# Performance work log

Hardware: AMD Instinct MI355X
Metric: run time of the kernel (lower is better)

The kernel has to match this reference:

```python
import jax, jax.numpy as jnp
import numpy as np

I4_CLIP = 7.0
NUM_HEADS = 16
NUM_KV_HEADS = 4
HEAD_DIM = 64
ROPE_BASE = 10000.0


def fake_quant_i4(w):
    # per-row int4 symmetric fake quantization with straight-through estimator
    row_max = jnp.maximum(jnp.max(jnp.abs(w), axis=-1, keepdims=True), 1e-8)
    scale = row_max / I4_CLIP
    w_deq = jnp.clip(jnp.round(w / scale), -I4_CLIP, I4_CLIP) * scale
    return w + jax.lax.stop_gradient(w_deq - w)


def rms_norm(x):
    eps = jnp.asarray(jnp.finfo(x.dtype).eps, x.dtype)
    return x * jax.lax.rsqrt(jnp.mean(x * x, axis=-1, keepdims=True) + eps)


def rope_cos_sin(seqlen, dtype):
    inv_freq = 1.0 / (ROPE_BASE ** (jnp.arange(0, HEAD_DIM, 2, dtype=jnp.float32) / HEAD_DIM))
    freqs = jnp.outer(jnp.arange(seqlen, dtype=jnp.float32), inv_freq)  # [S, hd/2]
    return jnp.cos(freqs).astype(dtype), jnp.sin(freqs).astype(dtype)


def apply_rotary(x, cos, sin):
    # x: [B, H, S, hd]; cos/sin: [S, hd/2] broadcast over B, H
    half = x.shape[-1] // 2
    x1, x2 = x[..., :half], x[..., half:]
    return jnp.concatenate((x1 * cos + x2 * sin, -x1 * sin + x2 * cos), axis=-1)


def setup_inputs() -> dict:
    key = jax.random.key(0)
    ks = jax.random.split(key, 6)
    dim = NUM_HEADS * HEAD_DIM
    kv_dim = NUM_KV_HEADS * HEAD_DIM
    return {
        "x": jax.random.normal(ks[0], (2, 2048, dim), jnp.float32),
        "w_q": jax.random.normal(ks[1], (dim, dim), jnp.float32) * 0.02,
        "w_k": jax.random.normal(ks[2], (kv_dim, dim), jnp.float32) * 0.02,
        "w_v": jax.random.normal(ks[3], (kv_dim, dim), jnp.float32) * 0.02,
        "w_proj": jax.random.normal(ks[4], (dim, dim), jnp.float32) * 0.02,
        "q_gain": jnp.ones((NUM_HEADS,), jnp.float32),
    }


def reference(x, w_q, w_k, w_v, w_proj, q_gain):
    bsz, seqlen, dim = x.shape
    rep = NUM_HEADS // NUM_KV_HEADS

    wq, wk, wv, wp = (fake_quant_i4(w) for w in (w_q, w_k, w_v, w_proj))

    # projections: F.linear(x, W) = x @ W.T -> [B, S, out]; split heads -> [B, H, S, hd]
    q = (x @ wq.T).reshape(bsz, seqlen, NUM_HEADS, HEAD_DIM).transpose(0, 2, 1, 3)
    k = (x @ wk.T).reshape(bsz, seqlen, NUM_KV_HEADS, HEAD_DIM).transpose(0, 2, 1, 3)
    v = (x @ wv.T).reshape(bsz, seqlen, NUM_KV_HEADS, HEAD_DIM).transpose(0, 2, 1, 3)

    q, k = rms_norm(q), rms_norm(k)
    cos, sin = rope_cos_sin(seqlen, q.dtype)
    q = apply_rotary(q, cos, sin)
    k = apply_rotary(k, cos, sin)
    q = q * q_gain.astype(q.dtype)[None, :, None, None]

    # GQA: expand kv heads
    k = jnp.repeat(k, rep, axis=1)
    v = jnp.repeat(v, rep, axis=1)

    # causal SDPA
    scale = 1.0 / np.sqrt(HEAD_DIM)
    scores = jnp.einsum("bhqd,bhkd->bhqk", q, k) * scale
    causal = jnp.tril(jnp.ones((seqlen, seqlen), dtype=bool))
    scores = jnp.where(causal, scores, jnp.asarray(-jnp.inf, scores.dtype))
    attn = jax.nn.softmax(scores, axis=-1)
    y = jnp.einsum("bhqk,bhkd->bhqd", attn, v)

    y = y.transpose(0, 2, 1, 3).reshape(bsz, seqlen, dim)
    return y @ wp.T
```

## Files before the change

kernel.cpp:

```cpp
#include <hip/hip_runtime.h>


typedef __bf16 bf16x8 __attribute__((ext_vector_type(8)));
typedef __bf16 bf16x4 __attribute__((ext_vector_type(4)));
typedef float  f32x4  __attribute__((ext_vector_type(4)));

__device__ __forceinline__ unsigned short f2bf(float f) {
  __bf16 h = (__bf16)f;
  return __builtin_bit_cast(unsigned short, h);
}

__global__ void quant_rows(const float* __restrict__ src,
                           unsigned short* __restrict__ dst, int ncols) {
  int row = blockIdx.x;
  const float* s = src + (size_t)row * ncols;
  unsigned short* d = dst + (size_t)row * ncols;
  int t = threadIdx.x;
  float v[4]; float mx = 0.f;
#pragma unroll
  for (int i = 0; i < 4; i++) { v[i] = s[t + 256 * i]; mx = fmaxf(mx, fabsf(v[i])); }
#pragma unroll
  for (int m = 1; m < 64; m <<= 1) mx = fmaxf(mx, __shfl_xor(mx, m));
  __shared__ float smx[4];
  if ((t & 63) == 0) smx[t >> 6] = mx;
  __syncthreads();
  mx = fmaxf(fmaxf(smx[0], smx[1]), fmaxf(smx[2], smx[3]));
  mx = fmaxf(mx, 1e-8f);
  float scale = mx / 7.0f;
#pragma unroll
  for (int i = 0; i < 4; i++) {
    float q = rintf(v[i] / scale);
    q = fminf(fmaxf(q, -7.0f), 7.0f);
    d[t + 256 * i] = f2bf(q * scale);
  }
}

__global__ void cvt_bf16(const float* __restrict__ src,
                         unsigned short* __restrict__ dst, int n) {
  int i = (blockIdx.x * 256 + threadIdx.x) * 4;
  if (i >= n) return;
  float4 f = *(const float4*)(src + i);
  ushort4 o;
  o.x = f2bf(f.x); o.y = f2bf(f.y); o.z = f2bf(f.z); o.w = f2bf(f.w);
  *(ushort4*)(dst + i) = o;
}

#define GLDS(g, l)                                                            \
  __builtin_amdgcn_global_load_lds((const __attribute__((address_space(1))) void*)(g), \
                                   (__attribute__((address_space(3))) void*)(l), 16, 0, 0)

__global__ __launch_bounds__(256, 2) void gemm_bt(
    const unsigned short* __restrict__ A, const unsigned short* __restrict__ Bw,
    float* __restrict__ C, int N, int K, int nbn) {
  int bm = blockIdx.x / nbn, bn = blockIdx.x % nbn;
  int tid = threadIdx.x, w = tid >> 6, lane = tid & 63;
  int l15 = lane & 15, lh = lane >> 4;
  __shared__ __align__(16) unsigned short ldsA[2][128 * 64];
  __shared__ __align__(16) unsigned short ldsB[2][128 * 64];
  int wr = w >> 1, wc = w & 1;
  f32x4 zero = {0.f, 0.f, 0.f, 0.f};
  f32x4 acc[4][4];
#pragma unroll
  for (int i = 0; i < 4; i++)
#pragma unroll
    for (int j = 0; j < 4; j++) acc[i][j] = zero;

  int srow = lane >> 3, schunk = (lane & 7) ^ (lane >> 3);
  const unsigned short* gA0 = A  + (size_t)(bm * 128 + srow) * K + schunk * 8;
  const unsigned short* gB0 = Bw + (size_t)(bn * 128 + srow) * K + schunk * 8;

  int nk = K >> 6;
#pragma unroll
  for (int it = 0; it < 4; it++) {
    int seg = w * 4 + it;
    GLDS(gA0 + (size_t)(seg * 8) * K, (unsigned short*)ldsA[0] + seg * 512);
    GLDS(gB0 + (size_t)(seg * 8) * K, (unsigned short*)ldsB[0] + seg * 512);
  }
  __syncthreads();
  int cur = 0;
  for (int kt = 0; kt < nk; kt++) {
    if (kt + 1 < nk) {
      int k0 = (kt + 1) * 64;
#pragma unroll
      for (int it = 0; it < 4; it++) {
        int seg = w * 4 + it;
        GLDS(gA0 + (size_t)(seg * 8) * K + k0, (unsigned short*)ldsA[cur ^ 1] + seg * 512);
        GLDS(gB0 + (size_t)(seg * 8) * K + k0, (unsigned short*)ldsB[cur ^ 1] + seg * 512);
      }
    }
    const unsigned short* cA = ldsA[cur];
    const unsigned short* cB = ldsB[cur];
#pragma unroll
    for (int ks = 0; ks < 2; ks++) {
      bf16x8 af[4], bfr[4];
#pragma unroll
      for (int fm = 0; fm < 4; fm++) {
        int row = wr * 64 + fm * 16 + l15;
        int slot = (ks * 4 + lh) ^ (row & 7);
        af[fm] = *(const bf16x8*)(cA + row * 64 + slot * 8);
      }
#pragma unroll
      for (int fn = 0; fn < 4; fn++) {
        int row = wc * 64 + fn * 16 + l15;
        int slot = (ks * 4 + lh) ^ (row & 7);
        bfr[fn] = *(const bf16x8*)(cB + row * 64 + slot * 8);
      }
#pragma unroll
      for (int fm = 0; fm < 4; fm++)
#pragma unroll
        for (int fn = 0; fn < 4; fn++)
          acc[fm][fn] = __builtin_amdgcn_mfma_f32_16x16x32_bf16(af[fm], bfr[fn], acc[fm][fn], 0, 0, 0);
    }
    __syncthreads();
    cur ^= 1;
  }
#pragma unroll
  for (int fm = 0; fm < 4; fm++) {
    int r0 = bm * 128 + wr * 64 + fm * 16 + lh * 4;
#pragma unroll
    for (int fn = 0; fn < 4; fn++) {
      int c = bn * 128 + wc * 64 + fn * 16 + l15;
#pragma unroll
      for (int reg = 0; reg < 4; reg++)
        C[(size_t)(r0 + reg) * N + c] = acc[fm][fn][reg];
    }
  }
}

__global__ __launch_bounds__(256, 2) void gemm_qkv(
    const unsigned short* __restrict__ A, const unsigned short* __restrict__ Bw,
    const float* __restrict__ gainp,
    unsigned short* __restrict__ qb, unsigned short* __restrict__ kbp,
    unsigned short* __restrict__ vbp) {
  const int K = 1024;
  int bm = blockIdx.x / 12, bn = blockIdx.x % 12;
  int tid = threadIdx.x, w = tid >> 6, lane = tid & 63;
  int l15 = lane & 15, lh = lane >> 4;
  __shared__ __align__(16) unsigned short ldsA[2][128 * 64];
  __shared__ __align__(16) unsigned short ldsB[2][128 * 64];
  int wr = w >> 1, wc = w & 1;
  f32x4 zero = {0.f, 0.f, 0.f, 0.f};
  f32x4 acc[4][4];
#pragma unroll
  for (int i = 0; i < 4; i++)
#pragma unroll
    for (int j = 0; j < 4; j++) acc[i][j] = zero;

  int srow = lane >> 3, schunk = (lane & 7) ^ (lane >> 3);
  const unsigned short* gA0 = A  + (size_t)(bm * 128 + srow) * K + schunk * 8;
  const unsigned short* gB0 = Bw + (size_t)(bn * 128 + srow) * K + schunk * 8;

#pragma unroll
  for (int it = 0; it < 4; it++) {
    int seg = w * 4 + it;
    GLDS(gA0 + (size_t)(seg * 8) * K, (unsigned short*)ldsA[0] + seg * 512);
    GLDS(gB0 + (size_t)(seg * 8) * K, (unsigned short*)ldsB[0] + seg * 512);
  }
  __syncthreads();
  int cur = 0;
  for (int kt = 0; kt < 16; kt++) {
    if (kt + 1 < 16) {
      int k0 = (kt + 1) * 64;
#pragma unroll
      for (int it = 0; it < 4; it++) {
        int seg = w * 4 + it;
        GLDS(gA0 + (size_t)(seg * 8) * K + k0, (unsigned short*)ldsA[cur ^ 1] + seg * 512);
        GLDS(gB0 + (size_t)(seg * 8) * K + k0, (unsigned short*)ldsB[cur ^ 1] + seg * 512);
      }
    }
    const unsigned short* cA = ldsA[cur];
    const unsigned short* cB = ldsB[cur];
#pragma unroll
    for (int ks = 0; ks < 2; ks++) {
      bf16x8 af[4], bfr[4];
#pragma unroll
      for (int fm = 0; fm < 4; fm++) {
        int row = wr * 64 + fm * 16 + l15;
        int slot = (ks * 4 + lh) ^ (row & 7);
        af[fm] = *(const bf16x8*)(cA + row * 64 + slot * 8);
      }
#pragma unroll
      for (int fn = 0; fn < 4; fn++) {
        int row = wc * 64 + fn * 16 + l15;
        int slot = (ks * 4 + lh) ^ (row & 7);
        bfr[fn] = *(const bf16x8*)(cB + row * 64 + slot * 8);
      }
#pragma unroll
      for (int fm = 0; fm < 4; fm++)
#pragma unroll
        for (int fn = 0; fn < 4; fn++)
          acc[fm][fn] = __builtin_amdgcn_mfma_f32_16x16x32_bf16(af[fm], bfr[fn], acc[fm][fn], 0, 0, 0);
    }
    __syncthreads();
    cur ^= 1;
  }

  int hid = bn * 2 + wc;
  int rbase = bm * 128 + wr * 64;
  if (hid >= 20) {
    int vh = hid - 20;
#pragma unroll
    for (int fm = 0; fm < 4; fm++)
#pragma unroll
      for (int reg = 0; reg < 4; reg++) {
        int r = rbase + fm * 16 + lh * 4 + reg;
        int b = r >> 11, s = r & 2047;
        unsigned short* dst = vbp + (((size_t)(b * 4 + vh) * 2048 + s) << 6);
#pragma unroll
        for (int fn = 0; fn < 4; fn++)
          dst[fn * 16 + l15] = f2bf(acc[fm][fn][reg]);
      }
  } else {
    bool isq = hid < 16;
    float gn = isq ? gainp[hid] : 1.0f;
    float invf0 = __expf(-0.28782313662425572f * (float)l15);
    float invf1 = __expf(-0.28782313662425572f * (float)(l15 + 16));
#pragma unroll
    for (int fm = 0; fm < 4; fm++)
#pragma unroll
      for (int reg = 0; reg < 4; reg++) {
        float y0 = acc[fm][0][reg], y1 = acc[fm][1][reg];
        float y2 = acc[fm][2][reg], y3 = acc[fm][3][reg];
        float ss = y0 * y0 + y1 * y1 + y2 * y2 + y3 * y3;
        ss += __shfl_xor(ss, 1); ss += __shfl_xor(ss, 2);
        ss += __shfl_xor(ss, 4); ss += __shfl_xor(ss, 8);
        float rn = rsqrtf(ss * 0.015625f + 1.1920929e-7f);
        y0 *= rn; y1 *= rn; y2 *= rn; y3 *= rn;
        int r = rbase + fm * 16 + lh * 4 + reg;
        int b = r >> 11, s = r & 2047;
        float c0, s0n, c1, s1n;
        __sincosf((float)s * invf0, &s0n, &c0);
        __sincosf((float)s * invf1, &s1n, &c1);
        float o0 = (y0 * c0 + y2 * s0n) * gn;
        float o1 = (y1 * c1 + y3 * s1n) * gn;
        float o2 = (y2 * c0 - y0 * s0n) * gn;
        float o3 = (y3 * c1 - y1 * s1n) * gn;
        unsigned short* dst = isq
          ? qb  + (((size_t)(b * 16 + hid) * 2048 + s) << 6)
          : kbp + (((size_t)(b * 4 + (hid - 16)) * 2048 + s) << 6);
        dst[l15]      = f2bf(o0);
        dst[l15 + 16] = f2bf(o1);
        dst[l15 + 32] = f2bf(o2);
        dst[l15 + 48] = f2bf(o3);
      }
  }
}

__global__ void v_transpose(const unsigned short* __restrict__ vbp,
                            unsigned short* __restrict__ vt) {
  int bid = blockIdx.x;
  int st = bid & 31, bk = bid >> 5;
  __shared__ unsigned short tile[64][72];
  int t = threadIdx.x;
  int sl = t >> 2, d0 = (t & 3) * 16;
  const unsigned short* src = vbp + (((size_t)bk * 2048 + st * 64 + sl) << 6) + d0;
  *(ushort4*)&tile[sl][d0]      = *(const ushort4*)(src);
  *(ushort4*)&tile[sl][d0 + 4]  = *(const ushort4*)(src + 4);
  *(ushort4*)&tile[sl][d0 + 8]  = *(const ushort4*)(src + 8);
  *(ushort4*)&tile[sl][d0 + 12] = *(const ushort4*)(src + 12);
  __syncthreads();
  int d = t >> 2, p0 = (t & 3) * 16;
  unsigned short* dst = vt + ((size_t)bk * 64 + d) * 2048 + st * 64 + p0;
#pragma unroll
  for (int jo = 0; jo < 16; jo += 4) {
    ushort4 a;
#pragma unroll
    for (int j = 0; j < 4; j++) {
      int p = p0 + jo + j;
      int c = ((p & 3) << 4) | (p >> 2);
      ((unsigned short*)&a)[j] = tile[c][d];
    }
    *(ushort4*)(dst + jo) = a;
  }
}

#define PSTR 72

template<bool MASK>
__device__ __forceinline__ void attn_tile(
    int kv0, int q0, int l15, int lh, float M2,
    const unsigned short* ldsK, const unsigned short* ldsV, unsigned short* pw,
    const bf16x8 (&qf)[2][2], float (&lsum)[2][4], f32x4 (&o)[2][4]) {
  const float K2 = 0.18033688011112042f;
  f32x4 zero = {0.f, 0.f, 0.f, 0.f};
  f32x4 sc[2][4];
#pragma unroll
  for (int fm = 0; fm < 2; fm++)
#pragma unroll
    for (int fn = 0; fn < 4; fn++) sc[fm][fn] = zero;
#pragma unroll
  for (int ks = 0; ks < 2; ks++) {
    bf16x8 kf[4];
#pragma unroll
    for (int fn = 0; fn < 4; fn++) {
      int row = fn * 16 + l15;
      int slot = (ks * 4 + lh) ^ (row & 7);
      kf[fn] = *(const bf16x8*)(ldsK + row * 64 + slot * 8);
    }
#pragma unroll
    for (int fm = 0; fm < 2; fm++)
#pragma unroll
      for (int fn = 0; fn < 4; fn++)
        sc[fm][fn] = __builtin_amdgcn_mfma_f32_16x16x32_bf16(qf[fm][ks], kf[fn], sc[fm][fn], 0, 0, 0);
  }
#pragma unroll
  for (int fm = 0; fm < 2; fm++)
#pragma unroll
    for (int r = 0; r < 4; r++) {
      bf16x4 pk;
      float ls = 0.f;
#pragma unroll
      for (int fn = 0; fn < 4; fn++) {
        float s = __builtin_fmaf(sc[fm][fn][r], K2, -M2);
        if (MASK) {
          int col = kv0 + fn * 16 + l15;
          int row = q0 + fm * 16 + lh * 4 + r;
          if (col > row) s = -1e30f;
        }
        float p = __builtin_amdgcn_exp2f(s);
        ls += p;
        pk[fn] = (__bf16)p;
      }
      *(bf16x4*)(pw + (fm * 16 + lh * 4 + r) * PSTR + l15 * 4) = pk;
      lsum[fm][r] += ls;
    }
  asm volatile("s_waitcnt lgkmcnt(0)" ::: "memory");
  __builtin_amdgcn_sched_barrier(0);
#pragma unroll
  for (int ks2 = 0; ks2 < 2; ks2++) {
    bf16x8 vf[4], pf[2];
#pragma unroll
    for (int fn = 0; fn < 4; fn++) {
      int row = fn * 16 + l15;
      int slot = (ks2 * 4 + lh) ^ (row & 7);
      vf[fn] = *(const bf16x8*)(ldsV + row * 64 + slot * 8);
    }
#pragma unroll
    for (int fm = 0; fm < 2; fm++)
      pf[fm] = *(const bf16x8*)(pw + (fm * 16 + l15) * PSTR + ks2 * 32 + lh * 8);
#pragma unroll
    for (int fm = 0; fm < 2; fm++)
#pragma unroll
      for (int fn = 0; fn < 4; fn++)
        o[fm][fn] = __builtin_amdgcn_mfma_f32_16x16x32_bf16(pf[fm], vf[fn], o[fm][fn], 0, 0, 0);
  }
}

__global__ __launch_bounds__(256, 3) void attn_fwd(
    const unsigned short* __restrict__ qbuf, const unsigned short* __restrict__ kb,
    const unsigned short* __restrict__ vtb, const float* __restrict__ gain,
    unsigned short* __restrict__ ob) {
  int bid = blockIdx.x;
  int g = bid >> 5;
  int qblk = (g < 8) ? (15 - g) : (g - 8);
  int bh = bid & 31;
  int b = bh >> 4, h = bh & 15;
  int tid = threadIdx.x;
  int w = tid >> 6, lane = tid & 63;
  int l15 = lane & 15, lh = lane >> 4;
  int q0 = qblk * 128 + w * 32;
  int kvh = h >> 2;
  const unsigned short* Q  = qbuf + (size_t)(b * 16 + h) * (2048 * 64);
  const unsigned short* Kg = kb   + (size_t)(b * 4 + kvh) * (2048 * 64);
  const unsigned short* Vg = vtb  + (size_t)(b * 4 + kvh) * (64 * 2048);

  __shared__ __align__(16) unsigned short ldsK[2][64 * 64];
  __shared__ __align__(16) unsigned short ldsV[2][64 * 64];
  __shared__ __align__(16) unsigned short plds[4][32 * PSTR];
  unsigned short* pw = plds[w];

  float gn = gain[h];
  float M2 = __builtin_fmaf(fabsf(gn), 1.46f, 0.02f);

  bf16x8 qf[2][2];
#pragma unroll
  for (int fm = 0; fm < 2; fm++)
#pragma unroll
    for (int ks = 0; ks < 2; ks++)
      qf[fm][ks] = *(const bf16x8*)(Q + (q0 + fm * 16 + l15) * 64 + ks * 32 + lh * 8);

  f32x4 zero = {0.f, 0.f, 0.f, 0.f};
  f32x4 o[2][4];
  float lsum[2][4];
#pragma unroll
  for (int fm = 0; fm < 2; fm++)
#pragma unroll
    for (int r = 0; r < 4; r++) { lsum[fm][r] = 0.f; o[fm][r] = zero; }

  int srow = lane >> 3;
  int schunk = (lane & 7) ^ (lane >> 3);
  int full = q0 >> 6;
  int nt = 2 * qblk + 2;

#pragma unroll
  for (int it = 0; it < 2; it++) {
    int seg = w * 2 + it;
    GLDS(Kg + (size_t)(seg * 8 + srow) * 64 + schunk * 8,
         (unsigned short*)ldsK[0] + seg * 512);
    GLDS(Vg + (size_t)(seg * 8 + srow) * 2048 + schunk * 8,
         (unsigned short*)ldsV[0] + seg * 512);
  }
  __syncthreads();
  int cur = 0;
  for (int t = 0; t < nt; t++) {
    int kv0 = t * 64;
    if (t + 1 < nt) {
      int kn = kv0 + 64;
#pragma unroll
      for (int it = 0; it < 2; it++) {
        int seg = w * 2 + it;
        GLDS(Kg + (size_t)(kn + seg * 8 + srow) * 64 + schunk * 8,
             (unsigned short*)ldsK[cur ^ 1] + seg * 512);
        GLDS(Vg + (size_t)(seg * 8 + srow) * 2048 + kn + schunk * 8,
             (unsigned short*)ldsV[cur ^ 1] + seg * 512);
      }
    }
    if (t < full)
      attn_tile<false>(kv0, q0, l15, lh, M2, ldsK[cur], ldsV[cur], pw, qf, lsum, o);
    else if (kv0 <= q0 + 31)
      attn_tile<true>(kv0, q0, l15, lh, M2, ldsK[cur], ldsV[cur], pw, qf, lsum, o);
    __syncthreads();
    cur ^= 1;
  }

#pragma unroll
  for (int fm = 0; fm < 2; fm++)
#pragma unroll
    for (int r = 0; r < 4; r++) {
      float l = lsum[fm][r];
      l += __shfl_xor(l, 1);
      l += __shfl_xor(l, 2);
      l += __shfl_xor(l, 4);
      l += __shfl_xor(l, 8);
      float inv = 1.0f / l;
      int row = q0 + fm * 16 + lh * 4 + r;
#pragma unroll
      for (int fn = 0; fn < 4; fn++) {
        int c = fn * 16 + l15;
        ob[(size_t)(b * 2048 + row) * 1024 + h * 64 + c] = f2bf(o[fm][fn][r] * inv);
      }
    }
}

extern "C" void kernel_launch(void* const* d_in, const int* in_sizes, int n_in,
                              void* d_out, int out_size, void* d_ws, size_t ws_size,
                              hipStream_t stream) {
  const float* x    = (const float*)d_in[0];
  const float* w_q  = (const float*)d_in[1];
  const float* w_k  = (const float*)d_in[2];
  const float* w_v  = (const float*)d_in[3];
  const float* w_p  = (const float*)d_in[4];
  const float* gain = (const float*)d_in[5];
  float* out = (float*)d_out;

  char* ws = (char*)d_ws;
  unsigned short* x_bf  = (unsigned short*)ws;
  unsigned short* wqkv  = (unsigned short*)(ws + (8u << 20));
  unsigned short* wp    = (unsigned short*)(ws + (11u << 20));
  unsigned short* qbuf  = (unsigned short*)(ws + (13u << 20));
  unsigned short* kbuf  = (unsigned short*)(ws + (21u << 20));
  unsigned short* vbuf  = (unsigned short*)(ws + (23u << 20));
  unsigned short* vtbuf = (unsigned short*)(ws + (25u << 20));
  unsigned short* aout  = (unsigned short*)(ws + (27u << 20));

  quant_rows<<<1024, 256, 0, stream>>>(w_q, wqkv, 1024);
  quant_rows<<<256, 256, 0, stream>>>(w_k, wqkv + 1024 * 1024, 1024);
  quant_rows<<<256, 256, 0, stream>>>(w_v, wqkv + 1280 * 1024, 1024);
  quant_rows<<<1024, 256, 0, stream>>>(w_p, wp, 1024);
  cvt_bf16<<<4096, 256, 0, stream>>>(x, x_bf, 4194304);
  gemm_qkv<<<32 * 12, 256, 0, stream>>>(x_bf, wqkv, gain, qbuf, kbuf, vbuf);
  v_transpose<<<256, 256, 0, stream>>>(vbuf, vtbuf);
  attn_fwd<<<512, 256, 0, stream>>>(qbuf, kbuf, vtbuf, gain, aout);
  gemm_bt<<<32 * 8, 256, 0, stream>>>(aout, wp, out, 1024, 1024, 8);
}
```

Baseline: 110.3 us.

## Split causal attention KV range across blocks and reduce partials in finalize kernel

Long query blocks now have their KV loop split into chunks of up to 8 tiles. Each chunk is handled by its own block, which writes unnormalized fp32 output and row sums to workspace. A new finalize kernel sums the partials and normalizes to bf16. The aim is to balance the causal triangle's uneven work across more blocks, at the cost of extra fp32 partial traffic and another kernel launch.

Result: slower. 114.8 us (+4.0%).

```diff
diff --git a/kernel.cpp b/kernel.cpp
--- a/kernel.cpp
+++ b/kernel.cpp
@@ -349,16 +349,26 @@
 __global__ __launch_bounds__(256, 3) void attn_fwd(
     const unsigned short* __restrict__ qbuf, const unsigned short* __restrict__ kb,
     const unsigned short* __restrict__ vtb, const float* __restrict__ gain,
-    unsigned short* __restrict__ ob) {
+    unsigned short* __restrict__ ob, float* __restrict__ pO,
+    float* __restrict__ pL) {
   int bid = blockIdx.x;
-  int g = bid >> 5;
-  int qblk = (g < 8) ? (15 - g) : (g - 8);
+  int cid = 39 - (bid >> 5);
   int bh = bid & 31;
   int b = bh >> 4, h = bh & 15;
+  int q, ch;
+  if (cid < 4)       { q = cid;             ch = 0; }
+  else if (cid < 12) { q = (cid + 4) >> 1;  ch = (cid + 4) & 1; }
+  else if (cid < 24) { q = (cid + 12) / 3;  ch = (cid + 12) % 3; }
+  else               { q = (cid + 24) >> 2; ch = (cid + 24) & 3; }
+  int nt = 2 * q + 2;
+  int t0 = ch * 8;
+  int t1 = (t0 + 8 < nt) ? t0 + 8 : nt;
+  bool direct = (cid < 4);
+
   int tid = threadIdx.x;
   int w = tid >> 6, lane = tid & 63;
   int l15 = lane & 15, lh = lane >> 4;
-  int q0 = qblk * 128 + w * 32;
+  int q0 = q * 128 + w * 32;
   int kvh = h >> 2;
   const unsigned short* Q  = qbuf + (size_t)(b * 16 + h) * (2048 * 64);
   const unsigned short* Kg = kb   + (size_t)(b * 4 + kvh) * (2048 * 64);
@@ -390,21 +400,20 @@
   int srow = lane >> 3;
   int schunk = (lane & 7) ^ (lane >> 3);
   int full = q0 >> 6;
-  int nt = 2 * qblk + 2;
 
 #pragma unroll
   for (int it = 0; it < 2; it++) {
     int seg = w * 2 + it;
-    GLDS(Kg + (size_t)(seg * 8 + srow) * 64 + schunk * 8,
+    GLDS(Kg + (size_t)(t0 * 64 + seg * 8 + srow) * 64 + schunk * 8,
          (unsigned short*)ldsK[0] + seg * 512);
-    GLDS(Vg + (size_t)(seg * 8 + srow) * 2048 + schunk * 8,
+    GLDS(Vg + (size_t)(seg * 8 + srow) * 2048 + t0 * 64 + schunk * 8,
          (unsigned short*)ldsV[0] + seg * 512);
   }
   __syncthreads();
   int cur = 0;
-  for (int t = 0; t < nt; t++) {
+  for (int t = t0; t < t1; t++) {
     int kv0 = t * 64;
-    if (t + 1 < nt) {
+    if (t + 1 < t1) {
       int kn = kv0 + 64;
 #pragma unroll
       for (int it = 0; it < 2; it++) {
@@ -423,23 +432,74 @@
     cur ^= 1;
   }
 
-#pragma unroll
-  for (int fm = 0; fm < 2; fm++)
-#pragma unroll
-    for (int r = 0; r < 4; r++) {
-      float l = lsum[fm][r];
-      l += __shfl_xor(l, 1);
-      l += __shfl_xor(l, 2);
-      l += __shfl_xor(l, 4);
-      l += __shfl_xor(l, 8);
-      float inv = 1.0f / l;
-      int row = q0 + fm * 16 + lh * 4 + r;
-#pragma unroll
-      for (int fn = 0; fn < 4; fn++) {
-        int c = fn * 16 + l15;
-        ob[(size_t)(b * 2048 + row) * 1024 + h * 64 + c] = f2bf(o[fm][fn][r] * inv);
-      }
-    }
+  if (direct) {
+#pragma unroll
+    for (int fm = 0; fm < 2; fm++)
+#pragma unroll
+      for (int r = 0; r < 4; r++) {
+        float l = lsum[fm][r];
+        l += __shfl_xor(l, 1); l += __shfl_xor(l, 2);
+        l += __shfl_xor(l, 4); l += __shfl_xor(l, 8);
+        float inv = 1.0f / l;
+        int row = q0 + fm * 16 + lh * 4 + r;
+#pragma unroll
+        for (int fn = 0; fn < 4; fn++)
+          ob[(size_t)(b * 2048 + row) * 1024 + h * 64 + fn * 16 + l15] =
+              f2bf(o[fm][fn][r] * inv);
+      }
+  } else {
+    int slot = bh * 36 + (cid - 4);
+    float* po = pO + ((size_t)slot << 13);
+    float* pl = pL + slot * 128;
+#pragma unroll
+    for (int fm = 0; fm < 2; fm++)
+#pragma unroll
+      for (int r = 0; r < 4; r++) {
+        float l = lsum[fm][r];
+        l += __shfl_xor(l, 1); l += __shfl_xor(l, 2);
+        l += __shfl_xor(l, 4); l += __shfl_xor(l, 8);
+        int row = w * 32 + fm * 16 + lh * 4 + r;
+        if (l15 == 0) pl[row] = l;
+#pragma unroll
+        for (int fn = 0; fn < 4; fn++)
+          po[row * 64 + fn * 16 + l15] = o[fm][fn][r];
+      }
+  }
+}
+
+__global__ __launch_bounds__(256) void attn_finalize(
+    const float* __restrict__ pO, const float* __restrict__ pL,
+    unsigned short* __restrict__ ob) {
+  int bid = blockIdx.x;
+  int q = 4 + (bid % 12);
+  int bh = bid / 12;
+  int b = bh >> 4, h = bh & 15;
+  int nc = (2 * q + 9) >> 3;
+  int cum = (q < 8) ? 2 * q - 4 : ((q < 12) ? 3 * q - 12 : 4 * q - 24);
+  int sbase = bh * 36 + (cum - 4);
+
+  int tid = threadIdx.x;
+  int row = tid >> 1, half = tid & 1;
+  f32x4 s[8];
+#pragma unroll
+  for (int j = 0; j < 8; j++) s[j] = (f32x4){0.f, 0.f, 0.f, 0.f};
+  float l = 0.f;
+  for (int c = 0; c < nc; c++) {
+    const float* po = pO + (((size_t)(sbase + c)) << 13) + row * 64 + half * 32;
+    l += pL[(sbase + c) * 128 + row];
+#pragma unroll
+    for (int j = 0; j < 8; j++) s[j] += *(const f32x4*)(po + j * 4);
+  }
+  float inv = 1.0f / l;
+  unsigned short* dst =
+      ob + (size_t)(b * 2048 + q * 128 + row) * 1024 + h * 64 + half * 32;
+#pragma unroll
+  for (int j = 0; j < 8; j++) {
+    ushort4 u;
+    u.x = f2bf(s[j][0] * inv); u.y = f2bf(s[j][1] * inv);
+    u.z = f2bf(s[j][2] * inv); u.w = f2bf(s[j][3] * inv);
+    *(ushort4*)(dst + j * 4) = u;
+  }
 }
 
 extern "C" void kernel_launch(void* const* d_in, const int* in_sizes, int n_in,
@@ -462,6 +522,8 @@
   unsigned short* vbuf  = (unsigned short*)(ws + (23u << 20));
   unsigned short* vtbuf = (unsigned short*)(ws + (25u << 20));
   unsigned short* aout  = (unsigned short*)(ws + (27u << 20));
+  float*          pO    = (float*)(ws + (35u << 20));
+  float*          pL    = (float*)(ws + (72u << 20));
 
   quant_rows<<<1024, 256, 0, stream>>>(w_q, wqkv, 1024);
   quant_rows<<<256, 256, 0, stream>>>(w_k, wqkv + 1024 * 1024, 1024);
@@ -470,6 +532,7 @@
   cvt_bf16<<<4096, 256, 0, stream>>>(x, x_bf, 4194304);
   gemm_qkv<<<32 * 12, 256, 0, stream>>>(x_bf, wqkv, gain, qbuf, kbuf, vbuf);
   v_transpose<<<256, 256, 0, stream>>>(vbuf, vtbuf);
-  attn_fwd<<<512, 256, 0, stream>>>(qbuf, kbuf, vtbuf, gain, aout);
+  attn_fwd<<<1280, 256, 0, stream>>>(qbuf, kbuf, vtbuf, gain, aout, pO, pL);
+  attn_finalize<<<384, 256, 0, stream>>>(pO, pL, aout);
   gemm_bt<<<32 * 8, 256, 0, stream>>>(aout, wp, out, 1024, 1024, 8);
 }
```
